# Optimization experiments

Measured on AMD Instinct MI355X. Metric: run time of the kernel, lower is better.

## Reference

```python
import jax, jax.numpy as jnp
import numpy as np

N, P, Q, T, J, B, H = 262144, 64, 64, 2048, 512, 8, 64


def setup_inputs() -> dict:
    key = jax.random.key(0)
    ks = jax.random.split(key, 11)
    sH = 1.0 / np.sqrt(H).astype(np.float32)
    return {
        "idx": jax.random.randint(ks[0], (B,), 0, J),
        "seg_ids": jnp.sort(jax.random.randint(ks[1], (N,), 0, T)),
        "K": jax.random.normal(ks[2], (N, P), jnp.float32) * 0.1,
        "V": jax.random.normal(ks[3], (N, Q), jnp.float32),
        "S": jax.random.normal(ks[4], (P, J), jnp.float32) * 0.1,
        "W_ih": jax.random.normal(ks[5], (3 * H, Q), jnp.float32) * sH,
        "W_hh": jax.random.normal(ks[6], (3 * H, H), jnp.float32) * sH,
        "b_ih": jax.random.normal(ks[7], (3 * H,), jnp.float32) * sH,
        "b_hh": jax.random.normal(ks[8], (3 * H,), jnp.float32) * sH,
        "w_out": jax.random.normal(ks[9], (1, H), jnp.float32) * sH,
        "b_out": jax.random.normal(ks[10], (1,), jnp.float32) * sH,
    }


def reference(idx, seg_ids, K, V, S, W_ih, W_hh, b_ih, b_hh, w_out, b_out):
    # W[:, b] = K @ S[:, idx[b]]  -> [N, B]
    w = K @ S[:, idx]
    # ragged per-segment softmax over the N axis (segments = date windows)
    m = jax.ops.segment_max(w, seg_ids, num_segments=T)          # [T, B]
    e = jnp.exp(w - m[seg_ids])                                  # [N, B]
    denom = jax.ops.segment_sum(e, seg_ids, num_segments=T)     # [T, B]
    alpha = e / denom[seg_ids]                                   # [N, B]
    # weighted aggregation of V rows per segment: M[t, b] = sum_u alpha_u * V_u
    M = jax.ops.segment_sum(alpha[:, :, None] * V[:, None, :],
                            seg_ids, num_segments=T)             # [T, B, Q]
    X = jnp.transpose(M, (1, 0, 2))                              # [B, T, Q]

    # PyTorch GRU (gate order r,z,n). Faithful to the original bug: GRU was
    # built without batch_first=True, so axis 0 (B) is time, axis 1 (T) is batch.
    def step(h, x_t):  # x_t: [T, Q], h: [T, H]
        gi = x_t @ W_ih.T + b_ih                                 # [T, 3H]
        gh = h @ W_hh.T + b_hh                                   # [T, 3H]
        i_r, i_z, i_n = jnp.split(gi, 3, axis=1)
        h_r, h_z, h_n = jnp.split(gh, 3, axis=1)
        r = jax.nn.sigmoid(i_r + h_r)
        z = jax.nn.sigmoid(i_z + h_z)
        n = jnp.tanh(i_n + r * h_n)
        h_new = (1.0 - z) * n + z * h
        return h_new, h_new

    h0 = jnp.zeros((T, H), X.dtype)
    _, hs = jax.lax.scan(step, h0, X)                            # [B, T, H]
    preds = hs @ w_out.T + b_out                                 # [B, T, 1]
    return preds
```

## Files before the change

kernel.cpp:

```cpp
#include <hip/hip_runtime.h>
#include <math.h>

#define NN 262144
#define PP 64
#define QQ 64
#define TT 2048
#define JJ 512
#define BB 8
#define HH 64

__device__ __forceinline__ float lane_bcast(float v, int l) {
  return __int_as_float(__builtin_amdgcn_readlane(__float_as_int(v), l));
}

__global__ void k_prep(const int* __restrict__ seg_ids, const int* __restrict__ idx,
                       const float* __restrict__ S, int* __restrict__ seg_start,
                       float* __restrict__ s_cols) {
  int tid = blockIdx.x * blockDim.x + threadIdx.x;
  if (tid <= TT) {
    int lo = 0, hi = NN;
    while (lo < hi) {
      int mid = (lo + hi) >> 1;
      int v = seg_ids[mid];
      if (v < tid) lo = mid + 1; else hi = mid;
    }
    seg_start[tid] = lo;
  }
  int t2 = tid - (TT + 1);
  if (t2 >= 0 && t2 < PP * BB) {
    int p = t2 >> 3, b = t2 & 7;
    s_cols[b * PP + p] = S[p * JJ + idx[b]];
  }
}

__global__ __launch_bounds__(256) void k_w(const float* __restrict__ Kmat,
                                           const float* __restrict__ s_cols,
                                           float* __restrict__ w) {
  __shared__ __align__(16) float s_lds[BB * PP];
  int tid = threadIdx.x;
  for (int i = tid; i < BB * PP; i += 256) s_lds[i] = s_cols[i];
  __syncthreads();
  int n = blockIdx.x * 64 + (tid >> 2);
  int sub = tid & 3;
  const float4* Kp = reinterpret_cast<const float4*>(Kmat + (size_t)n * PP + sub * 16);
  float4 kq[4];
#pragma unroll
  for (int j = 0; j < 4; ++j) kq[j] = Kp[j];
  float acc[8];
#pragma unroll
  for (int b = 0; b < 8; ++b) acc[b] = 0.f;
#pragma unroll
  for (int j4 = 0; j4 < 4; ++j4) {
    float4 kk = kq[j4];
#pragma unroll
    for (int b = 0; b < 8; ++b) {
      const float4 sv = *reinterpret_cast<const float4*>(&s_lds[b * PP + sub * 16 + j4 * 4]);
      acc[b] += kk.x * sv.x + kk.y * sv.y + kk.z * sv.z + kk.w * sv.w;
    }
  }
#pragma unroll
  for (int b = 0; b < 8; ++b) {
    acc[b] += __shfl_xor(acc[b], 1);
    acc[b] += __shfl_xor(acc[b], 2);
  }
  float ox = (sub == 0) ? acc[0] : (sub == 1) ? acc[2] : (sub == 2) ? acc[4] : acc[6];
  float oy = (sub == 0) ? acc[1] : (sub == 1) ? acc[3] : (sub == 2) ? acc[5] : acc[7];
  reinterpret_cast<float2*>(w + (size_t)n * 8)[sub] = make_float2(ox, oy);
}

__global__ __launch_bounds__(256) void k_seg(const float* __restrict__ w,
                                             const float* __restrict__ V,
                                             const int* __restrict__ seg_start,
                                             float* __restrict__ M) {
  __shared__ __align__(16) float alpha[64 * 8];
  __shared__ float accred[4][8][64];
  __shared__ float redm[4][8], reds[4][8];
  __shared__ float bcast[16];
  int t = blockIdx.x;
  int s = seg_start[t], e = seg_start[t + 1];
  int tid = threadIdx.x;
  int lane = tid & 63, wv = tid >> 6;

  float m[8];
#pragma unroll
  for (int b = 0; b < 8; ++b) m[b] = -INFINITY;
  for (int n = s + tid; n < e; n += 256) {
    const float4* wr = reinterpret_cast<const float4*>(w + (size_t)n * 8);
    float4 a0 = wr[0], a1 = wr[1];
    m[0] = fmaxf(m[0], a0.x); m[1] = fmaxf(m[1], a0.y);
    m[2] = fmaxf(m[2], a0.z); m[3] = fmaxf(m[3], a0.w);
    m[4] = fmaxf(m[4], a1.x); m[5] = fmaxf(m[5], a1.y);
    m[6] = fmaxf(m[6], a1.z); m[7] = fmaxf(m[7], a1.w);
  }
#pragma unroll
  for (int b = 0; b < 8; ++b) {
#pragma unroll
    for (int off = 1; off < 64; off <<= 1) m[b] = fmaxf(m[b], __shfl_xor(m[b], off));
  }
  if (lane == 0) {
#pragma unroll
    for (int b = 0; b < 8; ++b) redm[wv][b] = m[b];
  }
  __syncthreads();
  if (tid < 8) {
    bcast[tid] = fmaxf(fmaxf(redm[0][tid], redm[1][tid]),
                       fmaxf(redm[2][tid], redm[3][tid]));
  }
  __syncthreads();

  float mB = bcast[tid & 7];
  float se = 0.f;

  float acc[8];
#pragma unroll
  for (int b = 0; b < 8; ++b) acc[b] = 0.f;
  for (int base = s; base < e; base += 64) {
    int cnt = e - base; if (cnt > 64) cnt = 64;
    __syncthreads();
    for (int i = tid; i < cnt * 8; i += 256) {
      float ev = __expf(w[(size_t)base * 8 + i] - mB);
      alpha[i] = ev;
      se += ev;
    }
    __syncthreads();
    int rend = wv * 16 + 16; if (rend > cnt) rend = cnt;
    for (int r = wv * 16; r < rend; ++r) {
      float vv = V[(size_t)(base + r) * QQ + lane];
      const float4* al = reinterpret_cast<const float4*>(&alpha[r * 8]);
      float4 a0 = al[0], a1 = al[1];
      acc[0] += a0.x * vv; acc[1] += a0.y * vv; acc[2] += a0.z * vv; acc[3] += a0.w * vv;
      acc[4] += a1.x * vv; acc[5] += a1.y * vv; acc[6] += a1.z * vv; acc[7] += a1.w * vv;
    }
  }

  se += __shfl_xor(se, 8);
  se += __shfl_xor(se, 16);
  se += __shfl_xor(se, 32);
  __syncthreads();
  if (lane < 8) reds[wv][lane] = se;
#pragma unroll
  for (int b = 0; b < 8; ++b) accred[wv][b][lane] = acc[b];
  __syncthreads();
  if (tid < 8) {
    float dd = reds[0][tid] + reds[1][tid] + reds[2][tid] + reds[3][tid];
    bcast[8 + tid] = (dd > 0.f) ? 1.f / dd : 0.f;
  }
  __syncthreads();
  for (int o = tid; o < 512; o += 256) {
    int b = o >> 6, q = o & 63;
    float sum = accred[0][b][q] + accred[1][b][q] + accred[2][b][q] + accred[3][b][q];
    M[(size_t)t * 512 + o] = sum * bcast[8 + b];
  }
}

__global__ __launch_bounds__(256) void k_gi(const float* __restrict__ M,
                                            const float* __restrict__ W_ih,
                                            const float* __restrict__ b_ih,
                                            float* __restrict__ GI) {
  __shared__ float Wt[64 * 193];
  int tid = threadIdx.x;
  for (int i = tid; i < 192 * 64; i += 256) {
    int g = i >> 6, k = i & 63;
    Wt[k * 193 + g] = W_ih[i];
  }
  __syncthreads();
  int lane = tid & 63, wv = tid >> 6;
  int row0 = blockIdx.x * 32 + wv * 8;
  float x[8];
#pragma unroll
  for (int rr = 0; rr < 8; ++rr) {
    int rho = row0 + rr;
    int b = rho >> 11, t = rho & 2047;
    x[rr] = M[((size_t)t * 8 + b) * 64 + lane];
  }
  float bi0 = b_ih[lane], bi1 = b_ih[64 + lane], bi2 = b_ih[128 + lane];
  float a0[8], a1[8], a2[8];
#pragma unroll
  for (int rr = 0; rr < 8; ++rr) { a0[rr] = bi0; a1[rr] = bi1; a2[rr] = bi2; }
#pragma unroll
  for (int k = 0; k < 64; ++k) {
    float w0 = Wt[k * 193 + lane];
    float w1 = Wt[k * 193 + 64 + lane];
    float w2 = Wt[k * 193 + 128 + lane];
#pragma unroll
    for (int rr = 0; rr < 8; ++rr) {
      float xk = lane_bcast(x[rr], k);
      a0[rr] += w0 * xk; a1[rr] += w1 * xk; a2[rr] += w2 * xk;
    }
  }
#pragma unroll
  for (int rr = 0; rr < 8; ++rr) {
    size_t rho = (size_t)row0 + rr;
    GI[rho * 192 + lane]       = a0[rr];
    GI[rho * 192 + 64 + lane]  = a1[rr];
    GI[rho * 192 + 128 + lane] = a2[rr];
  }
}

__global__ __launch_bounds__(256) void k_gru(const float* __restrict__ GI,
                                             const float* __restrict__ W_hh,
                                             const float* __restrict__ b_hh,
                                             const float* __restrict__ w_out,
                                             const float* __restrict__ b_out,
                                             float* __restrict__ preds) {
  __shared__ float Wt[64 * 193];
  int tid = threadIdx.x;
  for (int i = tid; i < 192 * 64; i += 256) {
    int g = i >> 6, k = i & 63;
    Wt[k * 193 + g] = W_hh[i];
  }
  __syncthreads();
  int lane = tid & 63, wv = tid >> 6;
  int t = blockIdx.x * 4 + wv;
  float bh0 = b_hh[lane], bh1 = b_hh[64 + lane], bh2 = b_hh[128 + lane];
  float wo = w_out[lane];
  float bo = b_out[0];

  float gr[8], gz[8], gn[8];
#pragma unroll
  for (int b = 0; b < 8; ++b) {
    size_t base = ((size_t)b * TT + t) * 192;
    gr[b] = GI[base + lane];
    gz[b] = GI[base + 64 + lane];
    gn[b] = GI[base + 128 + lane];
  }

  float h;
  {
    float r = 1.f / (1.f + __expf(-(gr[0] + bh0)));
    float z = 1.f / (1.f + __expf(-(gz[0] + bh1)));
    float nv = tanhf(gn[0] + r * bh2);
    h = (1.f - z) * nv;
    float pv = h * wo;
#pragma unroll
    for (int off = 32; off; off >>= 1) pv += __shfl_xor(pv, off);
    if (lane == 0) preds[t] = pv + bo;
  }
#pragma unroll
  for (int b = 1; b < 8; ++b) {
    float ar = bh0, az = bh1, an = bh2;
#pragma unroll
    for (int k = 0; k < 64; ++k) {
      float hk = lane_bcast(h, k);
      float w0 = Wt[k * 193 + lane];
      float w1 = Wt[k * 193 + 64 + lane];
      float w2 = Wt[k * 193 + 128 + lane];
      ar += w0 * hk; az += w1 * hk; an += w2 * hk;
    }
    float r = 1.f / (1.f + __expf(-(gr[b] + ar)));
    float z = 1.f / (1.f + __expf(-(gz[b] + az)));
    float nv = tanhf(gn[b] + r * an);
    h = (1.f - z) * nv + z * h;
    float pv = h * wo;
#pragma unroll
    for (int off = 32; off; off >>= 1) pv += __shfl_xor(pv, off);
    if (lane == 0) preds[(size_t)b * TT + t] = pv + bo;
  }
}

extern "C" void kernel_launch(void* const* d_in, const int* in_sizes, int n_in,
                              void* d_out, int out_size, void* d_ws, size_t ws_size,
                              hipStream_t stream) {
  const int*   idx     = (const int*)d_in[0];
  const int*   seg_ids = (const int*)d_in[1];
  const float* Kmat    = (const float*)d_in[2];
  const float* V       = (const float*)d_in[3];
  const float* S       = (const float*)d_in[4];
  const float* W_ih    = (const float*)d_in[5];
  const float* W_hh    = (const float*)d_in[6];
  const float* b_ih    = (const float*)d_in[7];
  const float* b_hh    = (const float*)d_in[8];
  const float* w_out   = (const float*)d_in[9];
  const float* b_out   = (const float*)d_in[10];
  float* out = (float*)d_out;

  char* ws = (char*)d_ws;
  int*   seg_start = (int*)(ws + 0);
  float* s_cols    = (float*)(ws + 8448);
  float* w         = (float*)(ws + 10496);
  float* M         = (float*)(ws + 8399104);
  float* GI        = (float*)(ws + 12593408);

  hipLaunchKernelGGL(k_prep, dim3(11), dim3(256), 0, stream, seg_ids, idx, S, seg_start, s_cols);
  hipLaunchKernelGGL(k_w, dim3(NN / 64), dim3(256), 0, stream, Kmat, s_cols, w);
  hipLaunchKernelGGL(k_seg, dim3(TT), dim3(256), 0, stream, w, V, seg_start, M);
  hipLaunchKernelGGL(k_gi, dim3(512), dim3(256), 0, stream, M, W_ih, b_ih, GI);
  hipLaunchKernelGGL(k_gru, dim3(512), dim3(256), 0, stream, GI, W_hh, b_hh, w_out, b_out, out);
}
```

Baseline: 84.12 us.

## Vectorize segment V aggregation with float4 loads and 128-row chunks

Reworks the per-segment weighted V aggregation so each lane loads a float4 of V and handles 4 Q columns for 4 interleaved rows, with 32 accumulators per thread and a cross-lane shuffle reduction afterwards. The chunk size grows from 64 to 128 rows, which halves the number of barrier-separated chunks per segment. The goal is fewer, wider global loads and more independent FMAs per alpha read. In exchange it raises register pressure and adds shuffle reduction work, and segments average only about 128 rows, so the larger chunk may leave lanes idle.

```diff
diff --git a/kernel.cpp b/kernel.cpp
--- a/kernel.cpp
+++ b/kernel.cpp
@@ -72,7 +72,7 @@
                                              const float* __restrict__ V,
                                              const int* __restrict__ seg_start,
                                              float* __restrict__ M) {
-  __shared__ __align__(16) float alpha[64 * 8];
+  __shared__ __align__(16) float alpha[128 * 8];
   __shared__ float accred[4][8][64];
   __shared__ float redm[4][8], reds[4][8];
   __shared__ float bcast[16];
@@ -111,11 +111,14 @@
   float mB = bcast[tid & 7];
   float se = 0.f;
 
-  float acc[8];
-#pragma unroll
-  for (int b = 0; b < 8; ++b) acc[b] = 0.f;
-  for (int base = s; base < e; base += 64) {
-    int cnt = e - base; if (cnt > 64) cnt = 64;
+  int rsub = lane >> 4;
+  int qg = lane & 15;
+  float4 acc[8];
+#pragma unroll
+  for (int b = 0; b < 8; ++b) acc[b] = make_float4(0.f, 0.f, 0.f, 0.f);
+
+  for (int base = s; base < e; base += 128) {
+    int cnt = e - base; if (cnt > 128) cnt = 128;
     __syncthreads();
     for (int i = tid; i < cnt * 8; i += 256) {
       float ev = __expf(w[(size_t)base * 8 + i] - mB);
@@ -123,14 +126,31 @@
       se += ev;
     }
     __syncthreads();
-    int rend = wv * 16 + 16; if (rend > cnt) rend = cnt;
-    for (int r = wv * 16; r < rend; ++r) {
-      float vv = V[(size_t)(base + r) * QQ + lane];
-      const float4* al = reinterpret_cast<const float4*>(&alpha[r * 8]);
-      float4 a0 = al[0], a1 = al[1];
-      acc[0] += a0.x * vv; acc[1] += a0.y * vv; acc[2] += a0.z * vv; acc[3] += a0.w * vv;
-      acc[4] += a1.x * vv; acc[5] += a1.y * vv; acc[6] += a1.z * vv; acc[7] += a1.w * vv;
-    }
+#pragma unroll
+    for (int i = 0; i < 8; ++i) {
+      int r = wv * 32 + i * 4 + rsub;
+      if (r < cnt) {
+        float4 vv = reinterpret_cast<const float4*>(V + (size_t)(base + r) * QQ)[qg];
+        const float4* al = reinterpret_cast<const float4*>(&alpha[r * 8]);
+        float4 a0 = al[0], a1 = al[1];
+        acc[0].x += a0.x * vv.x; acc[0].y += a0.x * vv.y; acc[0].z += a0.x * vv.z; acc[0].w += a0.x * vv.w;
+        acc[1].x += a0.y * vv.x; acc[1].y += a0.y * vv.y; acc[1].z += a0.y * vv.z; acc[1].w += a0.y * vv.w;
+        acc[2].x += a0.z * vv.x; acc[2].y += a0.z * vv.y; acc[2].z += a0.z * vv.z; acc[2].w += a0.z * vv.w;
+        acc[3].x += a0.w * vv.x; acc[3].y += a0.w * vv.y; acc[3].z += a0.w * vv.z; acc[3].w += a0.w * vv.w;
+        acc[4].x += a1.x * vv.x; acc[4].y += a1.x * vv.y; acc[4].z += a1.x * vv.z; acc[4].w += a1.x * vv.w;
+        acc[5].x += a1.y * vv.x; acc[5].y += a1.y * vv.y; acc[5].z += a1.y * vv.z; acc[5].w += a1.y * vv.w;
+        acc[6].x += a1.z * vv.x; acc[6].y += a1.z * vv.y; acc[6].z += a1.z * vv.z; acc[6].w += a1.z * vv.w;
+        acc[7].x += a1.w * vv.x; acc[7].y += a1.w * vv.y; acc[7].z += a1.w * vv.z; acc[7].w += a1.w * vv.w;
+      }
+    }
+  }
+
+#pragma unroll
+  for (int b = 0; b < 8; ++b) {
+    acc[b].x += __shfl_xor(acc[b].x, 16); acc[b].y += __shfl_xor(acc[b].y, 16);
+    acc[b].z += __shfl_xor(acc[b].z, 16); acc[b].w += __shfl_xor(acc[b].w, 16);
+    acc[b].x += __shfl_xor(acc[b].x, 32); acc[b].y += __shfl_xor(acc[b].y, 32);
+    acc[b].z += __shfl_xor(acc[b].z, 32); acc[b].w += __shfl_xor(acc[b].w, 32);
   }
 
   se += __shfl_xor(se, 8);
@@ -138,8 +158,11 @@
   se += __shfl_xor(se, 32);
   __syncthreads();
   if (lane < 8) reds[wv][lane] = se;
-#pragma unroll
-  for (int b = 0; b < 8; ++b) accred[wv][b][lane] = acc[b];
+  if (rsub == 0) {
+#pragma unroll
+    for (int b = 0; b < 8; ++b)
+      *reinterpret_cast<float4*>(&accred[wv][b][qg * 4]) = acc[b];
+  }
   __syncthreads();
   if (tid < 8) {
     float dd = reds[0][tid] + reds[1][tid] + reds[2][tid] + reds[3][tid];
```

New measurement: 82.42 us. 2.0% less time.
